# Kernel tuning notes

Measured on AMD Instinct MI355X. Metric: run time of the kernel, lower is better.

The kernel has to match this reference:

```python
import jax, jax.numpy as jnp
import numpy as np

EPSILON = 1.5  # quality-tolerance threshold from init_kwargs
NEG_INF = -1000000000.0


def setup_inputs() -> dict:
    key = jax.random.key(0)
    k1, k2, k3 = jax.random.split(key, 3)
    B, S, D, E = 4, 4096, 2048, 64
    return {
        "hidden_states": jax.random.normal(k1, (B, S, D), dtype=jnp.float32),
        "gate_W": jax.random.normal(k2, (E, D), dtype=jnp.float32),  # nn.Linear weight [out,in]
        "secret_projection": jax.random.normal(k3, (D, E), dtype=jnp.float32),
        "top_k": 2,
    }


def reference(hidden_states, gate_W, secret_projection, top_k):
    # raw gate logits: Linear without bias -> x @ W^T
    raw_logits = jnp.einsum("bsd,ed->bse", hidden_states, gate_W)
    # watermark bias via secret LSH projection
    watermark_bias = jnp.einsum("bsd,de->bse", hidden_states, secret_projection)
    # indifference zone: experts whose logit is within epsilon of the max
    max_logits = jnp.max(raw_logits, axis=-1, keepdims=True)
    safe_mask = raw_logits >= max_logits - EPSILON
    modified_scores = jnp.where(safe_mask, watermark_bias, jnp.asarray(NEG_INF, raw_logits.dtype))
    # top-k over watermark-preferred safe experts
    _, selected_experts = jax.lax.top_k(modified_scores, top_k)
    # gather original logits at selected experts, softmax over the k slots
    router_logits = jnp.take_along_axis(raw_logits, selected_experts, axis=-1)
    routing_weights = jax.nn.softmax(router_logits, axis=-1)
    return routing_weights, selected_experts
```

## Files before the change

### kernel.cpp

```cpp
#include <hip/hip_runtime.h>
#include <stdint.h>


#define DDIM 2048
#define NEXP 64
#define NEG_INF  -1000000000.0f
#define MRG_RAW  0.04f
#define MRG_WM   0.15f

typedef __attribute__((ext_vector_type(8))) short bf16x8;
typedef __attribute__((ext_vector_type(4))) float f32x4;

union BFrag { bf16x8 v; uint32_t w[4]; uint4 q; };

__device__ inline void split8_rne(const float* a, bf16x8* hi, bf16x8* lo) {
    BFrag h, l;
    #pragma unroll
    for (int p = 0; p < 4; ++p) {
        const uint32_t u0 = __float_as_uint(a[2*p]);
        const uint32_t u1 = __float_as_uint(a[2*p+1]);
        const uint32_t h0 = (u0 + 0x7FFFu + ((u0 >> 16) & 1u)) >> 16;
        const uint32_t h1 = (u1 + 0x7FFFu + ((u1 >> 16) & 1u)) >> 16;
        const float r0 = a[2*p]   - __uint_as_float(h0 << 16);
        const float r1 = a[2*p+1] - __uint_as_float(h1 << 16);
        const uint32_t v0 = __float_as_uint(r0);
        const uint32_t v1 = __float_as_uint(r1);
        const uint32_t l0 = (v0 + 0x7FFFu + ((v0 >> 16) & 1u)) >> 16;
        const uint32_t l1 = (v1 + 0x7FFFu + ((v1 >> 16) & 1u)) >> 16;
        h.w[p] = h0 | (h1 << 16);
        l.w[p] = l0 | (l1 << 16);
    }
    *hi = h.v; *lo = l.v;
}

__device__ inline void split8t(const float* a, bf16x8* hi, bf16x8* lo) {
    BFrag h, l;
    #pragma unroll
    for (int p = 0; p < 4; ++p) {
        const uint32_t u0 = __float_as_uint(a[2*p]);
        const uint32_t u1 = __float_as_uint(a[2*p+1]);
        h.w[p] = (u0 >> 16) | (u1 & 0xFFFF0000u);
        const float r0 = a[2*p]   - __uint_as_float(u0 & 0xFFFF0000u);
        const float r1 = a[2*p+1] - __uint_as_float(u1 & 0xFFFF0000u);
        l.w[p] = (__float_as_uint(r0) >> 16) | (__float_as_uint(r1) & 0xFFFF0000u);
    }
    *hi = h.v; *lo = l.v;
}

__global__ void prep_b(const float* __restrict__ gateW, const float* __restrict__ secret,
                       uint4* __restrict__ wsB) {
    const int kstep = blockIdx.x;
    const int s = threadIdx.x >> 6;
    const int l = threadIdx.x & 63;
    const int col = s * 16 + (l & 15);
    const int kb  = kstep * 32 + (l >> 4) * 8;
    float v[8];
    if (col < NEXP) {
        #pragma unroll
        for (int j = 0; j < 8; ++j) v[j] = gateW[(size_t)col * DDIM + kb + j];
    } else {
        #pragma unroll
        for (int j = 0; j < 8; ++j) v[j] = secret[(size_t)(kb + j) * NEXP + (col - NEXP)];
    }
    bf16x8 hi, lo; split8_rne(v, &hi, &lo);
    const size_t base = (size_t)(kstep * 8 + s) * 128 + l;
    BFrag t;
    t.v = hi; wsB[base]      = t.q;
    t.v = lo; wsB[base + 64] = t.q;
}

__device__ inline void gl_lds16(const char* g, char* l) {
    __builtin_amdgcn_global_load_lds(
        (const __attribute__((address_space(1))) void*)g,
        (__attribute__((address_space(3))) void*)l, 16, 0, 0);
}

template <int KSPLIT>
__global__ __launch_bounds__(256, 4)
void gemm_q(const float* __restrict__ x, const char* __restrict__ wsB,
            float* __restrict__ wsP, int ntok)
{
    const int NTS = (DDIM / KSPLIT) / 32;
    __shared__ __align__(16) char lds[2][16384];

    const int tid = threadIdx.x;
    const int w = tid >> 6, l = tid & 63;
    const int c = l & 15;
    const int g = l >> 4;
    const int q  = blockIdx.x & (KSPLIT - 1);
    const int mb = blockIdx.x / KSPLIT;
    const int rowbase = mb * 64 + w * 16;

    f32x4 acc[8];
    #pragma unroll
    for (int s = 0; s < 8; ++s) acc[s] = (f32x4){0.f, 0.f, 0.f, 0.f};

    const float* xr = x + (size_t)(rowbase + c) * DDIM + q * (DDIM / KSPLIT) + g * 8;
    const char*  bq = wsB + (size_t)(q * NTS) * 16384;

    #define STAGE(ts, buf)                                                       \
        {                                                                        \
            _Pragma("unroll")                                                    \
            for (int j = 0; j < 4; ++j) {                                        \
                const int i = j * 4 + w;                                         \
                gl_lds16(bq + ((size_t)((ts) * 8 + (i >> 1)) * 128               \
                               + (i & 1) * 64 + l) * 16,                         \
                         &lds[buf][i * 1024 + l * 16]);                          \
            }                                                                    \
        }

    float4 A0a, A0b, A1a, A1b;
    STAGE(0, 0);
    A0a = *reinterpret_cast<const float4*>(xr);
    A0b = *reinterpret_cast<const float4*>(xr + 4);
    asm volatile("s_waitcnt vmcnt(0)" ::: "memory");
    __builtin_amdgcn_s_barrier();

    #pragma unroll 1
    for (int ts = 0; ts < NTS; ++ts) {
        const int cur = ts & 1;
        if (ts + 1 < NTS) {
            STAGE(ts + 1, cur ^ 1);
            A1a = *reinterpret_cast<const float4*>(xr + (ts + 1) * 32);
            A1b = *reinterpret_cast<const float4*>(xr + (ts + 1) * 32 + 4);
        }

        const float va[8] = {A0a.x, A0a.y, A0a.z, A0a.w, A0b.x, A0b.y, A0b.z, A0b.w};
        bf16x8 ah, al;
        split8t(va, &ah, &al);

        const char* bb = lds[cur];
        #pragma unroll
        for (int s = 0; s < 8; ++s) {
            const bf16x8 bh = *reinterpret_cast<const bf16x8*>(bb + (2*s)     * 1024 + l * 16);
            const bf16x8 bl = *reinterpret_cast<const bf16x8*>(bb + (2*s + 1) * 1024 + l * 16);
            acc[s] = __builtin_amdgcn_mfma_f32_16x16x32_bf16(ah, bh, acc[s], 0, 0, 0);
            acc[s] = __builtin_amdgcn_mfma_f32_16x16x32_bf16(ah, bl, acc[s], 0, 0, 0);
            acc[s] = __builtin_amdgcn_mfma_f32_16x16x32_bf16(al, bh, acc[s], 0, 0, 0);
        }

        asm volatile("s_waitcnt vmcnt(0)" ::: "memory");
        __builtin_amdgcn_s_barrier();
        A0a = A1a; A0b = A1b;
    }
    #undef STAGE

    const size_t MN = (size_t)ntok * 128;
    #pragma unroll
    for (int s = 0; s < 8; ++s)
        #pragma unroll
        for (int r = 0; r < 4; ++r)
            wsP[(size_t)q * MN + (size_t)(rowbase + g * 4 + r) * 128 + s * 16 + c] = acc[s][r];
}

template <int KSPLIT>
__global__ __launch_bounds__(256, 4)
void router_k(const float* __restrict__ wsP,
              const float* __restrict__ x,
              const float* __restrict__ gateW,
              const float* __restrict__ secret,
              float* __restrict__ out, int ntok)
{
    const int t = blockIdx.x * 4 + (threadIdx.x >> 6);
    const int e = threadIdx.x & 63;
    const size_t MN = (size_t)ntok * 128;

    float raw = 0.f, wm = 0.f;
    #pragma unroll
    for (int q = 0; q < KSPLIT; ++q) {
        raw += wsP[(size_t)q * MN + (size_t)t * 128 + e];
        wm  += wsP[(size_t)q * MN + (size_t)t * 128 + NEXP + e];
    }

    float rmax = raw;
    #pragma unroll
    for (int off = 32; off; off >>= 1) rmax = fmaxf(rmax, __shfl_xor(rmax, off));

    if (__any(fabsf(raw - (rmax - 1.5f)) < MRG_RAW)) {
        float s0 = 0.f, s1 = 0.f, s2 = 0.f, s3 = 0.f;
        const float4* xr = reinterpret_cast<const float4*>(x + (size_t)t * DDIM);
        const float4* wr = reinterpret_cast<const float4*>(gateW + (size_t)e * DDIM);
        for (int k = 0; k < DDIM / 4; ++k) {
            const float4 a = xr[k], b = wr[k];
            s0 = fmaf(a.x, b.x, s0); s1 = fmaf(a.y, b.y, s1);
            s2 = fmaf(a.z, b.z, s2); s3 = fmaf(a.w, b.w, s3);
        }
        raw = (s0 + s1) + (s2 + s3);
        rmax = raw;
        #pragma unroll
        for (int off = 32; off; off >>= 1) rmax = fmaxf(rmax, __shfl_xor(rmax, off));
    }

    const bool safe = (raw >= rmax - 1.5f);
    float m = safe ? wm : NEG_INF;

    float v1 = m; int e1 = e;
    #pragma unroll
    for (int off = 32; off; off >>= 1) {
        const float ov = __shfl_xor(v1, off); const int oi = __shfl_xor(e1, off);
        if (ov > v1 || (ov == v1 && oi < e1)) { v1 = ov; e1 = oi; }
    }
    float v2 = (e == e1) ? -3.0e38f : m; int e2 = e;
    #pragma unroll
    for (int off = 32; off; off >>= 1) {
        const float ov = __shfl_xor(v2, off); const int oi = __shfl_xor(e2, off);
        if (ov > v2 || (ov == v2 && oi < e2)) { v2 = ov; e2 = oi; }
    }
    float v3 = (e == e1 || e == e2) ? -3.0e38f : m; int e3 = e;
    #pragma unroll
    for (int off = 32; off; off >>= 1) {
        const float ov = __shfl_xor(v3, off); const int oi = __shfl_xor(e3, off);
        if (ov > v3 || (ov == v3 && oi < e3)) { v3 = ov; e3 = oi; }
    }

    const bool wmRisk = (v2 > NEG_INF + 1.0f && v1 - v2 < MRG_WM) ||
                        (v3 > NEG_INF + 1.0f && v2 - v3 < MRG_WM);
    if (__any(wmRisk)) {
        float s0 = 0.f, s1 = 0.f, s2 = 0.f, s3 = 0.f;
        const float* xr = x + (size_t)t * DDIM;
        for (int k = 0; k < DDIM; k += 4) {
            s0 = fmaf(xr[k + 0], secret[(size_t)(k + 0) * NEXP + e], s0);
            s1 = fmaf(xr[k + 1], secret[(size_t)(k + 1) * NEXP + e], s1);
            s2 = fmaf(xr[k + 2], secret[(size_t)(k + 2) * NEXP + e], s2);
            s3 = fmaf(xr[k + 3], secret[(size_t)(k + 3) * NEXP + e], s3);
        }
        m = safe ? ((s0 + s1) + (s2 + s3)) : NEG_INF;
        v1 = m; e1 = e;
        #pragma unroll
        for (int off = 32; off; off >>= 1) {
            const float ov = __shfl_xor(v1, off); const int oi = __shfl_xor(e1, off);
            if (ov > v1 || (ov == v1 && oi < e1)) { v1 = ov; e1 = oi; }
        }
        v2 = (e == e1) ? -3.0e38f : m; e2 = e;
        #pragma unroll
        for (int off = 32; off; off >>= 1) {
            const float ov = __shfl_xor(v2, off); const int oi = __shfl_xor(e2, off);
            if (ov > v2 || (ov == v2 && oi < e2)) { v2 = ov; e2 = oi; }
        }
    }

    const float l1 = __shfl(raw, e1);
    const float l2 = __shfl(raw, e2);

    if (e == 0) {
        const float mm = fmaxf(l1, l2);
        const float x1 = expf(l1 - mm), x2 = expf(l2 - mm);
        const float inv = 1.0f / (x1 + x2);
        out[(size_t)t * 2 + 0] = x1 * inv;
        out[(size_t)t * 2 + 1] = x2 * inv;
        out[(size_t)2 * ntok + t * 2 + 0] = (float)e1;
        out[(size_t)2 * ntok + t * 2 + 1] = (float)e2;
    }
}

extern "C" void kernel_launch(void* const* d_in, const int* in_sizes, int n_in,
                              void* d_out, int out_size, void* d_ws, size_t ws_size,
                              hipStream_t stream) {
    const float* x      = (const float*)d_in[0];
    const float* gateW  = (const float*)d_in[1];
    const float* secret = (const float*)d_in[2];
    float* out = (float*)d_out;

    const int ntok = in_sizes[0] / DDIM;
    uint4* wsB = (uint4*)d_ws;
    float* wsP = (float*)((char*)d_ws + (2u << 20));
    const size_t MN4 = (size_t)ntok * 128 * 4;

    prep_b<<<64, 512, 0, stream>>>(gateW, secret, wsB);

    if (ws_size >= (2u << 20) + 4 * MN4) {
        gemm_q<4><<<(ntok / 64) * 4, 256, 0, stream>>>(x, (const char*)wsB, wsP, ntok);
        router_k<4><<<ntok / 4, 256, 0, stream>>>(wsP, x, gateW, secret, out, ntok);
    } else {
        gemm_q<1><<<(ntok / 64), 256, 0, stream>>>(x, (const char*)wsB, wsP, ntok);
        router_k<1><<<ntok / 4, 256, 0, stream>>>(wsP, x, gateW, secret, out, ntok);
    }
}
```

Measured before the change: 94.84 us.

## Stage activation tiles through swizzled LDS with 512-thread 128-token blocks

The GEMM kernel now uses 512-thread blocks covering 128 tokens, so each staged weight tile in LDS is shared by twice as many rows. Activation tiles are loaded asynchronously into LDS via global_load_lds with an XOR swizzle, replacing per-thread register prefetch. The aim is to halve weight-tile traffic per token and make the x loads asynchronous and coalesced. In exchange LDS use per block doubles to 64KB, which may cut occupancy, the last iteration reloads the same tile redundantly, and the KSPLIT=1 fallback for small workspaces is removed.

```diff
diff --git a/kernel.cpp b/kernel.cpp
--- a/kernel.cpp
+++ b/kernel.cpp
@@ -4,6 +4,9 @@
 
 #define DDIM 2048
 #define NEXP 64
+#define TOKB 128
+#define KSPL 4
+#define NTS  16
 #define NEG_INF  -1000000000.0f
 #define MRG_RAW  0.04f
 #define MRG_WM   0.15f
@@ -75,57 +78,65 @@
         (__attribute__((address_space(3))) void*)l, 16, 0, 0);
 }
 
-template <int KSPLIT>
-__global__ __launch_bounds__(256, 4)
-void gemm_q(const float* __restrict__ x, const char* __restrict__ wsB,
+__global__ __launch_bounds__(512, 4)
+void gemm_p(const float* __restrict__ x, const char* __restrict__ wsB,
             float* __restrict__ wsP, int ntok)
 {
-    const int NTS = (DDIM / KSPLIT) / 32;
-    __shared__ __align__(16) char lds[2][16384];
+    __shared__ __align__(16) char lds[2][32768];
 
     const int tid = threadIdx.x;
     const int w = tid >> 6, l = tid & 63;
     const int c = l & 15;
     const int g = l >> 4;
-    const int q  = blockIdx.x & (KSPLIT - 1);
-    const int mb = blockIdx.x / KSPLIT;
-    const int rowbase = mb * 64 + w * 16;
+    const int q  = blockIdx.x & (KSPL - 1);
+    const int mb = blockIdx.x / KSPL;
+    const int rowbase = mb * TOKB;
+    const int wrow = rowbase + w * 16;
 
     f32x4 acc[8];
     #pragma unroll
     for (int s = 0; s < 8; ++s) acc[s] = (f32x4){0.f, 0.f, 0.f, 0.f};
 
-    const float* xr = x + (size_t)(rowbase + c) * DDIM + q * (DDIM / KSPLIT) + g * 8;
     const char*  bq = wsB + (size_t)(q * NTS) * 16384;
-
-    #define STAGE(ts, buf)                                                       \
-        {                                                                        \
-            _Pragma("unroll")                                                    \
-            for (int j = 0; j < 4; ++j) {                                        \
-                const int i = j * 4 + w;                                         \
-                gl_lds16(bq + ((size_t)((ts) * 8 + (i >> 1)) * 128               \
-                               + (i & 1) * 64 + l) * 16,                         \
-                         &lds[buf][i * 1024 + l * 16]);                          \
-            }                                                                    \
-        }
-
-    float4 A0a, A0b, A1a, A1b;
+    const float* xq = x + q * (DDIM / KSPL);
+
+    #define STAGE(ts, buf)                                                         \
+        {                                                                          \
+            _Pragma("unroll")                                                      \
+            for (int j = 0; j < 2; ++j) {                                          \
+                const int slot = j * 512 + tid;                                    \
+                const int i = slot >> 6;                                           \
+                gl_lds16(bq + (size_t)(ts) * 16384 + i * 1024 + l * 16,            \
+                         &lds[buf][slot * 16]);                                    \
+            }                                                                      \
+            _Pragma("unroll")                                                      \
+            for (int j = 0; j < 2; ++j) {                                          \
+                const int a = j * 512 + tid;                                       \
+                const int r = a >> 3, cg = a & 7;                                  \
+                const int scg = cg ^ (r & 7);                                      \
+                gl_lds16((const char*)(xq + (size_t)(rowbase + r) * DDIM           \
+                                       + (ts) * 32 + scg * 4),                     \
+                         &lds[buf][16384 + a * 16]);                               \
+            }                                                                      \
+        }
+
     STAGE(0, 0);
-    A0a = *reinterpret_cast<const float4*>(xr);
-    A0b = *reinterpret_cast<const float4*>(xr + 4);
     asm volatile("s_waitcnt vmcnt(0)" ::: "memory");
     __builtin_amdgcn_s_barrier();
 
     #pragma unroll 1
     for (int ts = 0; ts < NTS; ++ts) {
         const int cur = ts & 1;
-        if (ts + 1 < NTS) {
-            STAGE(ts + 1, cur ^ 1);
-            A1a = *reinterpret_cast<const float4*>(xr + (ts + 1) * 32);
-            A1b = *reinterpret_cast<const float4*>(xr + (ts + 1) * 32 + 4);
-        }
-
-        const float va[8] = {A0a.x, A0a.y, A0a.z, A0a.w, A0b.x, A0b.y, A0b.z, A0b.w};
+        const int nts = (ts + 1 < NTS) ? ts + 1 : ts;
+        STAGE(nts, cur ^ 1);
+
+        const char* ab = &lds[cur][16384];
+        const int r = w * 16 + c;
+        const int s0 = (2 * g)     ^ (r & 7);
+        const int s1 = (2 * g + 1) ^ (r & 7);
+        const float4 fa = *reinterpret_cast<const float4*>(ab + r * 128 + s0 * 16);
+        const float4 fb = *reinterpret_cast<const float4*>(ab + r * 128 + s1 * 16);
+        const float va[8] = {fa.x, fa.y, fa.z, fa.w, fb.x, fb.y, fb.z, fb.w};
         bf16x8 ah, al;
         split8t(va, &ah, &al);
 
@@ -141,7 +152,6 @@
 
         asm volatile("s_waitcnt vmcnt(0)" ::: "memory");
         __builtin_amdgcn_s_barrier();
-        A0a = A1a; A0b = A1b;
     }
     #undef STAGE
 
@@ -150,7 +160,7 @@
     for (int s = 0; s < 8; ++s)
         #pragma unroll
         for (int r = 0; r < 4; ++r)
-            wsP[(size_t)q * MN + (size_t)(rowbase + g * 4 + r) * 128 + s * 16 + c] = acc[s][r];
+            wsP[(size_t)q * MN + (size_t)(wrow + g * 4 + r) * 128 + s * 16 + c] = acc[s][r];
 }
 
 template <int KSPLIT>
@@ -264,15 +274,8 @@
     const int ntok = in_sizes[0] / DDIM;
     uint4* wsB = (uint4*)d_ws;
     float* wsP = (float*)((char*)d_ws + (2u << 20));
-    const size_t MN4 = (size_t)ntok * 128 * 4;
 
     prep_b<<<64, 512, 0, stream>>>(gateW, secret, wsB);
-
-    if (ws_size >= (2u << 20) + 4 * MN4) {
-        gemm_q<4><<<(ntok / 64) * 4, 256, 0, stream>>>(x, (const char*)wsB, wsP, ntok);
-        router_k<4><<<ntok / 4, 256, 0, stream>>>(wsP, x, gateW, secret, out, ntok);
-    } else {
-        gemm_q<1><<<(ntok / 64), 256, 0, stream>>>(x, (const char*)wsB, wsP, ntok);
-        router_k<1><<<ntok / 4, 256, 0, stream>>>(wsP, x, gateW, secret, out, ntok);
-    }
-}
+    gemm_p<<<(ntok / TOKB) * KSPL, 512, 0, stream>>>(x, (const char*)wsB, wsP, ntok);
+    router_k<KSPL><<<ntok / 4, 256, 0, stream>>>(wsP, x, gateW, secret, out, ntok);
+}
```

Result: no change. 94.86 us (median of 2 runs) (+0.0%).
